# Optimization experiments

Measured on AMD Instinct MI355X. Metric: run time of the kernel, lower is better.

## Reference

```python
import jax, jax.numpy as jnp
import numpy as np
import math

D = 1024
H = 16

def setup_inputs() -> dict:
    key = jax.random.key(0)
    ks = jax.random.split(key, 8)
    N, X, T = 2, 1024, 4096
    s = 1.0 / math.sqrt(D)
    return {
        "previous_output": jax.random.normal(ks[0], (N, X, D), jnp.float32),
        "context": jax.random.normal(ks[1], (N, T, D), jnp.float32),
        "Wq": jax.random.normal(ks[2], (D, D), jnp.float32) * s,
        "bq": jnp.zeros((D,), jnp.float32),
        "Wk": jax.random.normal(ks[3], (D, D), jnp.float32) * s,
        "bk": jnp.zeros((D,), jnp.float32),
        "Wv": jax.random.normal(ks[4], (D, D), jnp.float32) * s,
        "bv": jnp.zeros((D,), jnp.float32),
    }

def reference(previous_output, context, Wq, bq, Wk, bk, Wv, bv):
    N, X, _ = previous_output.shape
    T = context.shape[1]
    hd = D // H
    # linear projections (torch Linear: x @ W.T + b)
    q = (previous_output @ Wq.T + bq).reshape(N, X, H, hd).transpose(0, 2, 1, 3)  # (N,H,X,hd)
    k = (context @ Wk.T + bk).reshape(N, T, H, hd).transpose(0, 2, 1, 3)          # (N,H,T,hd)
    v = (context @ Wv.T + bv).reshape(N, T, H, hd).transpose(0, 2, 1, 3)          # (N,H,T,hd)
    scores = jnp.einsum('nhxd,nhtd->nhxt', q, k) / jnp.sqrt(jnp.float32(hd))       # (N,H,X,T)
    attn = jax.nn.softmax(scores, axis=-1)
    out = jnp.einsum('nhxt,nhtd->nhxd', attn, v)                                   # (N,H,X,hd)
    return out.transpose(0, 2, 1, 3).reshape(N, X, D)
```

## Files before the change

### kernel.cpp

```cpp
#include <hip/hip_runtime.h>

typedef __bf16 bf16_t;
typedef __bf16 bf16x8 __attribute__((ext_vector_type(8)));
typedef __bf16 bf16x4 __attribute__((ext_vector_type(4)));
typedef float f32x4 __attribute__((ext_vector_type(4)));

#define D_MODEL 1024
#define NHEAD 16
#define HD 64
#define XLEN 1024
#define TLEN 4096
#define NBATCH 2
#define CEXP 0.18033688011112042f

typedef __attribute__((address_space(3))) bf16_t lds_bf16;
typedef const __attribute__((address_space(1))) bf16_t glb_bf16;

__global__ __launch_bounds__(256) void convert5(const float* __restrict__ prev, const float* __restrict__ ctx,
                                                const float* __restrict__ wq, const float* __restrict__ wk,
                                                const float* __restrict__ wv,
                                                bf16_t* __restrict__ prev_b, bf16_t* __restrict__ ctx_b,
                                                bf16_t* __restrict__ wq_b, bf16_t* __restrict__ wk_b,
                                                bf16_t* __restrict__ wv_b) {
    int b = blockIdx.x;
    const float* src; bf16_t* dst; int lb;
    if (b < 256)       { src = prev; dst = prev_b; lb = b; }
    else if (b < 1280) { src = ctx;  dst = ctx_b;  lb = b - 256; }
    else if (b < 1408) { src = wq;   dst = wq_b;   lb = b - 1280; }
    else if (b < 1536) { src = wk;   dst = wk_b;   lb = b - 1408; }
    else               { src = wv;   dst = wv_b;   lb = b - 1536; }
    const int base = lb * 8192 + threadIdx.x * 4;
#pragma unroll
    for (int i = 0; i < 8; ++i) {
        const int off = base + i * 1024;
        f32x4 f = *(const f32x4*)(src + off);
        bf16x4 h;
        h[0] = (bf16_t)f[0]; h[1] = (bf16_t)f[1]; h[2] = (bf16_t)f[2]; h[3] = (bf16_t)f[3];
        *(bf16x4*)(dst + off) = h;
    }
}

__global__ __launch_bounds__(256) void gemm_fused(const bf16_t* __restrict__ Xq, const bf16_t* __restrict__ Xc,
                                                  const bf16_t* __restrict__ wq, const bf16_t* __restrict__ wk,
                                                  const bf16_t* __restrict__ wv,
                                                  const float* __restrict__ bq, const float* __restrict__ bk,
                                                  const float* __restrict__ bv,
                                                  bf16_t* __restrict__ Qh, bf16_t* __restrict__ Kh,
                                                  bf16_t* __restrict__ Vt) {
    __shared__ bf16_t Ab[128][32];
    __shared__ bf16_t Bb[128][32];

    const int tid  = threadIdx.x;
    const int w    = tid >> 6;
    const int lane = tid & 63;
    const int q4   = lane >> 4;
    const int c    = lane & 15;

    const bf16_t* X; const bf16_t* W; const float* bias;
    int m0, n0, lshift, vmode;
    const int bid = blockIdx.x;
    if (bid < 128) {
        X = Xq; W = wq; bias = bq; lshift = 10; vmode = 0;
        m0 = (bid >> 3) * 128; n0 = (bid & 7) * 128;
    } else {
        const int b = bid - 128;
        const int xcd  = b & 7;
        const int s    = b >> 3;
        const int nb   = s >> 3;
        const int mgrp = s & 7;
        m0 = (mgrp * 8 + xcd) * 128;
        X = Xc; lshift = 12;
        if (nb < 8) { W = wk; bias = bk; vmode = 0; n0 = nb * 128; }
        else        { W = wv; bias = bv; vmode = 1; n0 = (nb - 8) * 128; }
    }
    const float osc = (bid < 128) ? CEXP : 1.0f;

    f32x4 acc[4][4];
#pragma unroll
    for (int i = 0; i < 4; ++i)
#pragma unroll
        for (int j = 0; j < 4; ++j) acc[i][j] = (f32x4){0.f, 0.f, 0.f, 0.f};

    const int mq = (w & 1) * 64;
    const int nq = (w >> 1) * 64;

    bf16_t* aBase = &Ab[0][0] + w * 512;
    bf16_t* bBase = &Bb[0][0] + w * 512;
    const bf16_t* gA = X + (size_t)(m0 + (tid >> 2)) * D_MODEL + (tid & 3) * 8;
    const bf16_t* gB = W + (size_t)(n0 + (tid >> 2)) * D_MODEL + (tid & 3) * 8;

    for (int kk = 0; kk < D_MODEL; kk += 32) {
        __syncthreads();
        __builtin_amdgcn_global_load_lds((glb_bf16*)(gA + kk), (lds_bf16*)aBase, 16, 0, 0);
        __builtin_amdgcn_global_load_lds((glb_bf16*)(gA + kk + (size_t)64 * D_MODEL), (lds_bf16*)(aBase + 2048), 16, 0, 0);
        __builtin_amdgcn_global_load_lds((glb_bf16*)(gB + kk), (lds_bf16*)bBase, 16, 0, 0);
        __builtin_amdgcn_global_load_lds((glb_bf16*)(gB + kk + (size_t)64 * D_MODEL), (lds_bf16*)(bBase + 2048), 16, 0, 0);
        __syncthreads();

        bf16x8 a[4], b[4];
#pragma unroll
        for (int i = 0; i < 4; ++i) a[i] = *(const bf16x8*)&Ab[mq + i * 16 + c][q4 * 8];
#pragma unroll
        for (int i = 0; i < 4; ++i) b[i] = *(const bf16x8*)&Bb[nq + i * 16 + c][q4 * 8];
#pragma unroll
        for (int mi = 0; mi < 4; ++mi)
#pragma unroll
            for (int ni = 0; ni < 4; ++ni)
                acc[mi][ni] = __builtin_amdgcn_mfma_f32_16x16x32_bf16(a[mi], b[ni], acc[mi][ni], 0, 0, 0);
    }

    float bv4[4];
#pragma unroll
    for (int ni = 0; ni < 4; ++ni) bv4[ni] = bias[n0 + nq + ni * 16 + c];

    const int headbase = (n0 + nq) >> 6;
    if (vmode == 0) {
        bf16_t* OutQK = (bid < 128) ? Qh : Kh;
        const int L = 1 << lshift;
#pragma unroll
        for (int mi = 0; mi < 4; ++mi) {
            const int mrow = m0 + mq + mi * 16 + q4 * 4;
            const int nb2  = mrow >> lshift;
            const int pos  = mrow & (L - 1);
            bf16_t* ob = OutQK + ((size_t)(nb2 * NHEAD + headbase) * L + pos) * HD;
#pragma unroll
            for (int ni = 0; ni < 4; ++ni) {
                const int d = ni * 16 + c;
#pragma unroll
                for (int r = 0; r < 4; ++r)
                    ob[(size_t)r * HD + d] = (bf16_t)((acc[mi][ni][r] + bv4[ni]) * osc);
            }
        }
    } else {
#pragma unroll
        for (int mi = 0; mi < 4; ++mi) {
            const int mrow = m0 + mq + mi * 16 + q4 * 4;
            const int nb2  = mrow >> 12;
            const int pos  = mrow & 4095;
            const int lin  = (pos & ~31) + ((pos >> 2) & 3) * 8 + ((pos >> 4) & 1) * 4;
#pragma unroll
            for (int ni = 0; ni < 4; ++ni) {
                const int d = ni * 16 + c;
                bf16x4 v4;
#pragma unroll
                for (int r = 0; r < 4; ++r) v4[r] = (bf16_t)(acc[mi][ni][r] + bv4[ni]);
                *(bf16x4*)(Vt + ((size_t)(nb2 * NHEAD + headbase) * HD + d) * TLEN + lin) = v4;
            }
        }
    }
}

__global__ __launch_bounds__(256, 4) void attn_kernel(const bf16_t* __restrict__ Qh,
                                                      const bf16_t* __restrict__ Kh,
                                                      const bf16_t* __restrict__ Vt,
                                                      bf16_t* __restrict__ Opart,
                                                      float* __restrict__ Lpart) {
    __shared__ __align__(16) char smem[32768];

    const int tid  = threadIdx.x;
    const int lane = tid & 63;
    const int w    = tid >> 6;
    const int q4   = lane >> 4;
    const int c    = lane & 15;

    const int bid = blockIdx.x;
    const int xcd = bid & 7;
    const int seq = bid >> 3;
    const int tq  = seq & 3;
    const int xb  = (seq >> 2) & 7;
    const int g   = seq >> 5;
    const int nh  = g * 8 + xcd;
    const int xw  = xb * 128 + w * 32;

    const bf16_t* __restrict__ Kb = Kh + (size_t)nh * TLEN * HD;
    const bf16_t* __restrict__ Vb = Vt + (size_t)nh * HD * TLEN;

    bf16x8 qa[2][2];
#pragma unroll
    for (int mi = 0; mi < 2; ++mi) {
        const bf16_t* qr = Qh + ((size_t)nh * XLEN + xw + mi * 16 + c) * HD + q4 * 8;
        qa[mi][0] = *(const bf16x8*)(qr);
        qa[mi][1] = *(const bf16x8*)(qr + 32);
    }

    const int sRow0 = tid >> 3,  sRow1 = 32 + (tid >> 3);
    const int sCh   = tid & 7;
    const int kCol0 = ((sCh ^ (sRow0 & 7)) * 8);
    const int kCol1 = ((sCh ^ (sRow1 & 7)) * 8);

    const int ofs0 = c * 128 + ((q4 ^ (c & 7)) * 16);
    const int ofs1 = c * 128 + (((4 + q4) ^ (c & 7)) * 16);

    f32x4 o[2][4];
#pragma unroll
    for (int i = 0; i < 2; ++i)
#pragma unroll
        for (int j = 0; j < 4; ++j) o[i][j] = (f32x4){0.f, 0.f, 0.f, 0.f};
    f32x4 lacc[2];
    lacc[0] = (f32x4){0.f, 0.f, 0.f, 0.f};
    lacc[1] = (f32x4){0.f, 0.f, 0.f, 0.f};

    bf16x8 ones8;
#pragma unroll
    for (int j = 0; j < 8; ++j) ones8[j] = (bf16_t)1.0f;

    const int t0base = tq * (TLEN / 4);

    {
        bf16_t* base = (bf16_t*)smem;
        __builtin_amdgcn_global_load_lds((glb_bf16*)(Kb + (size_t)(t0base + sRow0) * HD + kCol0), (lds_bf16*)(base + w * 512), 16, 0, 0);
        __builtin_amdgcn_global_load_lds((glb_bf16*)(Kb + (size_t)(t0base + sRow1) * HD + kCol1), (lds_bf16*)(base + 2048 + w * 512), 16, 0, 0);
        __builtin_amdgcn_global_load_lds((glb_bf16*)(Vb + (size_t)sRow0 * TLEN + t0base + kCol0), (lds_bf16*)(base + 4096 + w * 512), 16, 0, 0);
        __builtin_amdgcn_global_load_lds((glb_bf16*)(Vb + (size_t)sRow1 * TLEN + t0base + kCol1), (lds_bf16*)(base + 6144 + w * 512), 16, 0, 0);
    }

    for (int s = 0; s < 16; ++s) {
        __syncthreads();
        if (s < 15) {
            const int t1 = t0base + (s + 1) * 64;
            bf16_t* base = (bf16_t*)smem + ((s + 1) & 1) * 8192;
            __builtin_amdgcn_global_load_lds((glb_bf16*)(Kb + (size_t)(t1 + sRow0) * HD + kCol0), (lds_bf16*)(base + w * 512), 16, 0, 0);
            __builtin_amdgcn_global_load_lds((glb_bf16*)(Kb + (size_t)(t1 + sRow1) * HD + kCol1), (lds_bf16*)(base + 2048 + w * 512), 16, 0, 0);
            __builtin_amdgcn_global_load_lds((glb_bf16*)(Vb + (size_t)sRow0 * TLEN + t1 + kCol0), (lds_bf16*)(base + 4096 + w * 512), 16, 0, 0);
            __builtin_amdgcn_global_load_lds((glb_bf16*)(Vb + (size_t)sRow1 * TLEN + t1 + kCol1), (lds_bf16*)(base + 6144 + w * 512), 16, 0, 0);
        }

        const char* KtB = smem + (s & 1) * 16384;
        const char* VsB = KtB + 8192;
#pragma unroll
        for (int g32 = 0; g32 < 2; ++g32) {
            bf16x8 p8[2];
#pragma unroll
            for (int tt = 0; tt < 2; ++tt) {
                const int rofs = g32 * 4096 + tt * 2048;
                bf16x8 kb0 = *(const bf16x8*)(KtB + rofs + ofs0);
                bf16x8 kb1 = *(const bf16x8*)(KtB + rofs + ofs1);
#pragma unroll
                for (int mi = 0; mi < 2; ++mi) {
                    f32x4 sv = (f32x4){0.f, 0.f, 0.f, 0.f};
                    sv = __builtin_amdgcn_mfma_f32_16x16x32_bf16(kb0, qa[mi][0], sv, 0, 0, 0);
                    sv = __builtin_amdgcn_mfma_f32_16x16x32_bf16(kb1, qa[mi][1], sv, 0, 0, 0);
#pragma unroll
                    for (int r = 0; r < 4; ++r)
                        p8[mi][tt * 4 + r] = (bf16_t)__builtin_exp2f(sv[r]);
                }
            }
            const int vsel = g32 ? ofs1 : ofs0;
            bf16x8 va[4];
#pragma unroll
            for (int dt = 0; dt < 4; ++dt)
                va[dt] = *(const bf16x8*)(VsB + vsel + dt * 2048);
#pragma unroll
            for (int mi = 0; mi < 2; ++mi) {
#pragma unroll
                for (int dt = 0; dt < 4; ++dt)
                    o[mi][dt] = __builtin_amdgcn_mfma_f32_16x16x32_bf16(va[dt], p8[mi], o[mi][dt], 0, 0, 0);
                lacc[mi] = __builtin_amdgcn_mfma_f32_16x16x32_bf16(ones8, p8[mi], lacc[mi], 0, 0, 0);
            }
        }
    }

    __syncthreads();
    bf16_t* Ob = (bf16_t*)smem;
    float*  Lb = (float*)(smem + 16896);
#pragma unroll
    for (int mi = 0; mi < 2; ++mi) {
        if (q4 == 0) Lb[w * 32 + mi * 16 + c] = lacc[mi][0];
#pragma unroll
        for (int dt = 0; dt < 4; ++dt)
#pragma unroll
            for (int r = 0; r < 4; ++r)
                Ob[w * 2112 + (dt * 16 + q4 * 4 + r) * 33 + mi * 16 + c] = (bf16_t)o[mi][dt][r];
    }
    {
        const int lr = lane >> 1;
        const int dh = lane & 1;
        bf16x8 out4[4];
#pragma unroll
        for (int j2 = 0; j2 < 4; ++j2)
#pragma unroll
            for (int e = 0; e < 8; ++e)
                out4[j2][e] = Ob[w * 2112 + (dh * 32 + j2 * 8 + e) * 33 + lr];
        const size_t pair = (size_t)nh * XLEN + xw + lr;
        bf16_t* op = Opart + (pair * 4 + tq) * HD + dh * 32;
#pragma unroll
        for (int j2 = 0; j2 < 4; ++j2)
            *(bf16x8*)(op + j2 * 8) = out4[j2];
        if (dh == 0) Lpart[pair * 4 + tq] = Lb[w * 32 + lr];
    }
}

__global__ __launch_bounds__(256) void attn_merge(const bf16_t* __restrict__ Opart,
                                                  const float* __restrict__ Lpart,
                                                  float* __restrict__ Out) {
    const int u    = blockIdx.x * 256 + threadIdx.x;
    const int pair = u >> 3;
    const int d0   = (u & 7) * 8;
    const int nh   = pair >> 10;
    const int x    = pair & 1023;
    const int n    = nh >> 4;
    const int h    = nh & 15;

    float l = 0.f;
    float s[8];
#pragma unroll
    for (int j = 0; j < 8; ++j) s[j] = 0.f;
#pragma unroll
    for (int tqi = 0; tqi < 4; ++tqi) {
        l += Lpart[pair * 4 + tqi];
        bf16x8 v = *(const bf16x8*)(Opart + ((size_t)pair * 4 + tqi) * HD + d0);
#pragma unroll
        for (int j = 0; j < 8; ++j) s[j] += (float)v[j];
    }
    const float inv = 1.0f / l;
    f32x4 v0, v1;
#pragma unroll
    for (int j = 0; j < 4; ++j) { v0[j] = s[j] * inv; v1[j] = s[4 + j] * inv; }
    float* op = Out + ((size_t)(n * XLEN + x)) * D_MODEL + h * HD + d0;
    *(f32x4*)(op)     = v0;
    *(f32x4*)(op + 4) = v1;
}

extern "C" void kernel_launch(void* const* d_in, const int* in_sizes, int n_in,
                              void* d_out, int out_size, void* d_ws, size_t ws_size,
                              hipStream_t stream) {
    (void)in_sizes; (void)n_in; (void)out_size; (void)ws_size;
    const float* prev = (const float*)d_in[0];
    const float* ctx  = (const float*)d_in[1];
    const float* Wq   = (const float*)d_in[2];
    const float* bq   = (const float*)d_in[3];
    const float* Wk   = (const float*)d_in[4];
    const float* bk   = (const float*)d_in[5];
    const float* Wv   = (const float*)d_in[6];
    const float* bv   = (const float*)d_in[7];

    const size_t MiB = 1024 * 1024;
    char* ws = (char*)d_ws;
    bf16_t* prev_b = (bf16_t*)(ws);
    bf16_t* ctx_b  = (bf16_t*)(ws + 4 * MiB);
    bf16_t* wq_b   = (bf16_t*)(ws + 20 * MiB);
    bf16_t* wk_b   = (bf16_t*)(ws + 22 * MiB);
    bf16_t* wv_b   = (bf16_t*)(ws + 24 * MiB);
    bf16_t* Qh     = (bf16_t*)(ws + 26 * MiB);
    bf16_t* Kh     = (bf16_t*)(ws + 30 * MiB);
    bf16_t* Vt     = (bf16_t*)(ws + 46 * MiB);
    bf16_t* Opart  = ctx_b;
    float*  Lpart  = (float*)prev_b;

    convert5<<<1664, 256, 0, stream>>>(prev, ctx, Wq, Wk, Wv, prev_b, ctx_b, wq_b, wk_b, wv_b);
    gemm_fused<<<128 + 1024, 256, 0, stream>>>(prev_b, ctx_b, wq_b, wk_b, wv_b, bq, bk, bv, Qh, Kh, Vt);
    attn_kernel<<<1024, 256, 0, stream>>>(Qh, Kh, Vt, Opart, Lpart);
    attn_merge<<<1024, 256, 0, stream>>>(Opart, Lpart, (float*)d_out);
}
```

Baseline: 207.8 us.

## Rewrite QKV projection GEMM with larger tiles and multi-stage LDS pipeline

```diff
diff --git a/kernel.cpp b/kernel.cpp
--- a/kernel.cpp
+++ b/kernel.cpp
@@ -15,6 +15,8 @@
 
 typedef __attribute__((address_space(3))) bf16_t lds_bf16;
 typedef const __attribute__((address_space(1))) bf16_t glb_bf16;
+
+#define MEMFENCE() asm volatile("" ::: "memory")
 
 __global__ __launch_bounds__(256) void convert5(const float* __restrict__ prev, const float* __restrict__ ctx,
                                                 const float* __restrict__ wq, const float* __restrict__ wk,
@@ -40,111 +42,205 @@
     }
 }
 
-__global__ __launch_bounds__(256) void gemm_fused(const bf16_t* __restrict__ Xq, const bf16_t* __restrict__ Xc,
-                                                  const bf16_t* __restrict__ wq, const bf16_t* __restrict__ wk,
-                                                  const bf16_t* __restrict__ wv,
-                                                  const float* __restrict__ bq, const float* __restrict__ bk,
-                                                  const float* __restrict__ bv,
-                                                  bf16_t* __restrict__ Qh, bf16_t* __restrict__ Kh,
-                                                  bf16_t* __restrict__ Vt) {
-    __shared__ bf16_t Ab[128][32];
-    __shared__ bf16_t Bb[128][32];
-
+template<int MF>
+__device__ __forceinline__ void gemm_core(const bf16_t* __restrict__ Xa,
+                                          const bf16_t* __restrict__ Wb,
+                                          int m0, int n0, char* smem,
+                                          f32x4 (&acc)[MF][4]) {
     const int tid  = threadIdx.x;
     const int w    = tid >> 6;
     const int lane = tid & 63;
     const int q4   = lane >> 4;
     const int c    = lane & 15;
-
-    const bf16_t* X; const bf16_t* W; const float* bias;
-    int m0, n0, lshift, vmode;
-    const int bid = blockIdx.x;
-    if (bid < 128) {
-        X = Xq; W = wq; bias = bq; lshift = 10; vmode = 0;
-        m0 = (bid >> 3) * 128; n0 = (bid & 7) * 128;
+    const int wm   = w >> 2;
+    const int wn   = w & 3;
+
+    constexpr int ABYTES = MF * 2048;
+    constexpr int BUFSZ  = ABYTES + 16384;
+    constexpr int AINSTR = MF / 4;
+    constexpr int NT     = 32;
+
+#pragma unroll
+    for (int i = 0; i < MF; ++i)
+#pragma unroll
+        for (int j = 0; j < 4; ++j) acc[i][j] = (f32x4){0.f, 0.f, 0.f, 0.f};
+
+    const int xp = ((lane & 3) * 16) ^ (((lane >> 5) & 1) << 5);
+    const char* gA = (const char*)Xa + ((size_t)(m0 + w * 16 + (lane >> 2)) << 11) + xp;
+    const char* gB = (const char*)Wb + ((size_t)(n0 + w * 16 + (lane >> 2)) << 11) + xp;
+    char* lw = smem + w * 1024;
+
+    const int fo = c * 64 + ((q4 * 16) ^ (((c >> 3) & 1) << 5));
+
+#pragma unroll
+    for (int t = 0; t < 3; ++t) {
+#pragma unroll
+        for (int i = 0; i < AINSTR; ++i)
+            __builtin_amdgcn_global_load_lds((glb_bf16*)(gA + (size_t)i * 262144 + t * 64),
+                                             (lds_bf16*)(lw + t * BUFSZ + i * 8192), 16, 0, 0);
+#pragma unroll
+        for (int i = 0; i < 2; ++i)
+            __builtin_amdgcn_global_load_lds((glb_bf16*)(gB + (size_t)i * 262144 + t * 64),
+                                             (lds_bf16*)(lw + t * BUFSZ + ABYTES + i * 8192), 16, 0, 0);
+        MEMFENCE();
+    }
+
+#pragma unroll 1
+    for (int t = 0; t < NT; ++t) {
+        if (t < NT - 2) {
+            if constexpr (AINSTR == 2) asm volatile("s_waitcnt vmcnt(8)" ::: "memory");
+            else                       asm volatile("s_waitcnt vmcnt(6)" ::: "memory");
+        } else if (t == NT - 2) {
+            if constexpr (AINSTR == 2) asm volatile("s_waitcnt vmcnt(4)" ::: "memory");
+            else                       asm volatile("s_waitcnt vmcnt(3)" ::: "memory");
+        } else {
+            asm volatile("s_waitcnt vmcnt(0)" ::: "memory");
+        }
+        __builtin_amdgcn_s_barrier();
+        MEMFENCE();
+
+        const char* cbuf = smem + (t & 3) * BUFSZ;
+        char* pbuf = lw + ((t + 3) & 3) * BUFSZ;
+        const bool pf = (t + 3) < NT;
+        const int tk = (t + 3) * 64;
+
+        if (pf) {
+#pragma unroll
+            for (int i = 0; i < AINSTR; ++i)
+                __builtin_amdgcn_global_load_lds((glb_bf16*)(gA + (size_t)i * 262144 + tk),
+                                                 (lds_bf16*)(pbuf + i * 8192), 16, 0, 0);
+        }
+        bf16x8 bfrag[4];
+#pragma unroll
+        for (int ni = 0; ni < 4; ++ni)
+            bfrag[ni] = *(const bf16x8*)(cbuf + ABYTES + (wn * 4 + ni) * 1024 + fo);
+        bf16x8 afrag[MF / 2];
+#pragma unroll
+        for (int mi = 0; mi < MF / 2; ++mi)
+            afrag[mi] = *(const bf16x8*)(cbuf + (wm * MF + mi) * 1024 + fo);
+        __builtin_amdgcn_s_setprio(1);
+#pragma unroll
+        for (int mi = 0; mi < MF / 2; ++mi)
+#pragma unroll
+            for (int ni = 0; ni < 4; ++ni)
+                acc[mi][ni] = __builtin_amdgcn_mfma_f32_16x16x32_bf16(afrag[mi], bfrag[ni], acc[mi][ni], 0, 0, 0);
+        __builtin_amdgcn_s_setprio(0);
+        MEMFENCE();
+        __builtin_amdgcn_s_barrier();
+        MEMFENCE();
+
+        if (pf) {
+#pragma unroll
+            for (int i = 0; i < 2; ++i)
+                __builtin_amdgcn_global_load_lds((glb_bf16*)(gB + (size_t)i * 262144 + tk),
+                                                 (lds_bf16*)(pbuf + ABYTES + i * 8192), 16, 0, 0);
+        }
+        bf16x8 afrag2[MF / 2];
+#pragma unroll
+        for (int mi = 0; mi < MF / 2; ++mi)
+            afrag2[mi] = *(const bf16x8*)(cbuf + (wm * MF + MF / 2 + mi) * 1024 + fo);
+        __builtin_amdgcn_s_setprio(1);
+#pragma unroll
+        for (int mi = 0; mi < MF / 2; ++mi)
+#pragma unroll
+            for (int ni = 0; ni < 4; ++ni)
+                acc[MF / 2 + mi][ni] = __builtin_amdgcn_mfma_f32_16x16x32_bf16(afrag2[mi], bfrag[ni], acc[MF / 2 + mi][ni], 0, 0, 0);
+        __builtin_amdgcn_s_setprio(0);
+        MEMFENCE();
+    }
+}
+
+__global__ __launch_bounds__(512, 2) void gemm_fused2(
+    const bf16_t* __restrict__ Xq, const bf16_t* __restrict__ Xc,
+    const bf16_t* __restrict__ wq, const bf16_t* __restrict__ wk, const bf16_t* __restrict__ wv,
+    const float* __restrict__ bq, const float* __restrict__ bk, const float* __restrict__ bv,
+    bf16_t* __restrict__ Qh, bf16_t* __restrict__ Kh, bf16_t* __restrict__ Vt) {
+    __shared__ __align__(16) char smem[131072];
+    const int bid  = blockIdx.x;
+    const int tid  = threadIdx.x;
+    const int w    = tid >> 6;
+    const int lane = tid & 63;
+    const int q4   = lane >> 4;
+    const int c    = lane & 15;
+    const int wm   = w >> 2;
+    const int wn   = w & 3;
+
+    if (bid < 256) {
+        const int xcd   = bid & 7;
+        const int vmode = xcd >> 2;
+        const int n0    = (xcd & 3) * 256;
+        const int m0    = (bid >> 3) * 256;
+        const bf16_t* W   = vmode ? wv : wk;
+        const float* bias = vmode ? bv : bk;
+
+        const int Nw = n0 + wn * 64;
+        float bz[4];
+#pragma unroll
+        for (int ni = 0; ni < 4; ++ni) bz[ni] = bias[Nw + ni * 16 + c];
+        MEMFENCE();
+
+        f32x4 acc[8][4];
+        gemm_core<8>(Xc, W, m0, n0, smem, acc);
+
+        const int Mw = m0 + wm * 128;
+        const int headbase = Nw >> 6;
+        if (vmode == 0) {
+#pragma unroll
+            for (int mi = 0; mi < 8; ++mi) {
+                const int mrow = Mw + mi * 16 + q4 * 4;
+                const int nb2 = mrow >> 12, pos = mrow & 4095;
+                bf16_t* ob = Kh + ((size_t)(nb2 * NHEAD + headbase) * TLEN + pos) * HD;
+#pragma unroll
+                for (int ni = 0; ni < 4; ++ni) {
+                    const int d = ni * 16 + c;
+#pragma unroll
+                    for (int r = 0; r < 4; ++r)
+                        ob[(size_t)r * HD + d] = (bf16_t)(acc[mi][ni][r] + bz[ni]);
+                }
+            }
+        } else {
+#pragma unroll
+            for (int mi = 0; mi < 8; ++mi) {
+                const int mrow = Mw + mi * 16 + q4 * 4;
+                const int nb2 = mrow >> 12, pos = mrow & 4095;
+                const int lin = (pos & ~31) + ((pos >> 2) & 3) * 8 + ((pos >> 4) & 1) * 4;
+#pragma unroll
+                for (int ni = 0; ni < 4; ++ni) {
+                    const int d = ni * 16 + c;
+                    bf16x4 v4;
+#pragma unroll
+                    for (int r = 0; r < 4; ++r) v4[r] = (bf16_t)(acc[mi][ni][r] + bz[ni]);
+                    *(bf16x4*)(Vt + ((size_t)(nb2 * NHEAD + headbase) * HD + d) * TLEN + lin) = v4;
+                }
+            }
+        }
     } else {
-        const int b = bid - 128;
-        const int xcd  = b & 7;
-        const int s    = b >> 3;
-        const int nb   = s >> 3;
-        const int mgrp = s & 7;
-        m0 = (mgrp * 8 + xcd) * 128;
-        X = Xc; lshift = 12;
-        if (nb < 8) { W = wk; bias = bk; vmode = 0; n0 = nb * 128; }
-        else        { W = wv; bias = bv; vmode = 1; n0 = (nb - 8) * 128; }
-    }
-    const float osc = (bid < 128) ? CEXP : 1.0f;
-
-    f32x4 acc[4][4];
-#pragma unroll
-    for (int i = 0; i < 4; ++i)
-#pragma unroll
-        for (int j = 0; j < 4; ++j) acc[i][j] = (f32x4){0.f, 0.f, 0.f, 0.f};
-
-    const int mq = (w & 1) * 64;
-    const int nq = (w >> 1) * 64;
-
-    bf16_t* aBase = &Ab[0][0] + w * 512;
-    bf16_t* bBase = &Bb[0][0] + w * 512;
-    const bf16_t* gA = X + (size_t)(m0 + (tid >> 2)) * D_MODEL + (tid & 3) * 8;
-    const bf16_t* gB = W + (size_t)(n0 + (tid >> 2)) * D_MODEL + (tid & 3) * 8;
-
-    for (int kk = 0; kk < D_MODEL; kk += 32) {
-        __syncthreads();
-        __builtin_amdgcn_global_load_lds((glb_bf16*)(gA + kk), (lds_bf16*)aBase, 16, 0, 0);
-        __builtin_amdgcn_global_load_lds((glb_bf16*)(gA + kk + (size_t)64 * D_MODEL), (lds_bf16*)(aBase + 2048), 16, 0, 0);
-        __builtin_amdgcn_global_load_lds((glb_bf16*)(gB + kk), (lds_bf16*)bBase, 16, 0, 0);
-        __builtin_amdgcn_global_load_lds((glb_bf16*)(gB + kk + (size_t)64 * D_MODEL), (lds_bf16*)(bBase + 2048), 16, 0, 0);
-        __syncthreads();
-
-        bf16x8 a[4], b[4];
-#pragma unroll
-        for (int i = 0; i < 4; ++i) a[i] = *(const bf16x8*)&Ab[mq + i * 16 + c][q4 * 8];
-#pragma unroll
-        for (int i = 0; i < 4; ++i) b[i] = *(const bf16x8*)&Bb[nq + i * 16 + c][q4 * 8];
-#pragma unroll
-        for (int mi = 0; mi < 4; ++mi)
-#pragma unroll
-            for (int ni = 0; ni < 4; ++ni)
-                acc[mi][ni] = __builtin_amdgcn_mfma_f32_16x16x32_bf16(a[mi], b[ni], acc[mi][ni], 0, 0, 0);
-    }
-
-    float bv4[4];
-#pragma unroll
-    for (int ni = 0; ni < 4; ++ni) bv4[ni] = bias[n0 + nq + ni * 16 + c];
-
-    const int headbase = (n0 + nq) >> 6;
-    if (vmode == 0) {
-        bf16_t* OutQK = (bid < 128) ? Qh : Kh;
-        const int L = 1 << lshift;
+        const int b  = bid - 256;
+        const int m0 = (b >> 2) * 128;
+        const int n0 = (b & 3) * 256;
+
+        const int Nw = n0 + wn * 64;
+        float bz[4];
+#pragma unroll
+        for (int ni = 0; ni < 4; ++ni) bz[ni] = bq[Nw + ni * 16 + c];
+        MEMFENCE();
+
+        f32x4 acc[4][4];
+        gemm_core<4>(Xq, wq, m0, n0, smem, acc);
+
+        const int Mw = m0 + wm * 64;
+        const int headbase = Nw >> 6;
 #pragma unroll
         for (int mi = 0; mi < 4; ++mi) {
-            const int mrow = m0 + mq + mi * 16 + q4 * 4;
-            const int nb2  = mrow >> lshift;
-            const int pos  = mrow & (L - 1);
-            bf16_t* ob = OutQK + ((size_t)(nb2 * NHEAD + headbase) * L + pos) * HD;
+            const int mrow = Mw + mi * 16 + q4 * 4;
+            const int nb2 = mrow >> 10, pos = mrow & 1023;
+            bf16_t* ob = Qh + ((size_t)(nb2 * NHEAD + headbase) * XLEN + pos) * HD;
 #pragma unroll
             for (int ni = 0; ni < 4; ++ni) {
                 const int d = ni * 16 + c;
 #pragma unroll
                 for (int r = 0; r < 4; ++r)
-                    ob[(size_t)r * HD + d] = (bf16_t)((acc[mi][ni][r] + bv4[ni]) * osc);
-            }
-        }
-    } else {
-#pragma unroll
-        for (int mi = 0; mi < 4; ++mi) {
-            const int mrow = m0 + mq + mi * 16 + q4 * 4;
-            const int nb2  = mrow >> 12;
-            const int pos  = mrow & 4095;
-            const int lin  = (pos & ~31) + ((pos >> 2) & 3) * 8 + ((pos >> 4) & 1) * 4;
-#pragma unroll
-            for (int ni = 0; ni < 4; ++ni) {
-                const int d = ni * 16 + c;
-                bf16x4 v4;
-#pragma unroll
-                for (int r = 0; r < 4; ++r) v4[r] = (bf16_t)(acc[mi][ni][r] + bv4[ni]);
-                *(bf16x4*)(Vt + ((size_t)(nb2 * NHEAD + headbase) * HD + d) * TLEN + lin) = v4;
+                    ob[(size_t)r * HD + d] = (bf16_t)((acc[mi][ni][r] + bz[ni]) * CEXP);
             }
         }
     }
@@ -348,7 +444,7 @@
     float*  Lpart  = (float*)prev_b;
 
     convert5<<<1664, 256, 0, stream>>>(prev, ctx, Wq, Wk, Wv, prev_b, ctx_b, wq_b, wk_b, wv_b);
-    gemm_fused<<<128 + 1024, 256, 0, stream>>>(prev_b, ctx_b, wq_b, wk_b, wv_b, bq, bk, bv, Qh, Kh, Vt);
+    gemm_fused2<<<320, 512, 0, stream>>>(prev_b, ctx_b, wq_b, wk_b, wv_b, bq, bk, bv, Qh, Kh, Vt);
     attn_kernel<<<1024, 256, 0, stream>>>(Qh, Kh, Vt, Opart, Lpart);
     attn_merge<<<1024, 256, 0, stream>>>(Opart, Lpart, (float*)d_out);
 }
```

Measured after the change: 204.9 us. No clear change (-1.4%).
